# Kernel tuning notes

Measured on AMD Instinct MI355X. Metric: run time of the kernel, lower is better.

## Reference

```python
import jax, jax.numpy as jnp
import numpy as np

NUM_NODES = 50000
EMB_DIM = 128
PROJ_DIM = 768
HIDDEN = 256
NUM_REL = 16
NUM_BASES = 2
NUM_LAYERS = 3
NUM_EDGES = 400000
BN_EPS = 1e-5


def setup_inputs() -> dict:
    key = jax.random.key(0)
    ks = jax.random.split(key, 32)
    inp = {}
    inp["edge_index"] = jax.random.randint(ks[0], (2, NUM_EDGES), 0, NUM_NODES)
    inp["edge_type"] = jax.random.randint(ks[1], (NUM_EDGES,), 0, NUM_REL)
    inp["emb"] = jax.random.normal(ks[2], (NUM_NODES, EMB_DIM), jnp.float32)
    inp["proj_w"] = jax.random.normal(ks[3], (EMB_DIM, PROJ_DIM), jnp.float32) * 0.02
    inp["proj_b"] = jnp.zeros((PROJ_DIM,), jnp.float32)
    dims_in = [PROJ_DIM, HIDDEN, HIDDEN]
    for l in range(NUM_LAYERS):
        d_in = dims_in[l]
        k0, k1, k2 = jax.random.split(ks[4 + l], 3)
        inp[f"comp{l}"] = jax.random.normal(k0, (NUM_REL, NUM_BASES), jnp.float32)
        inp[f"bases{l}"] = jax.random.normal(k1, (NUM_BASES, d_in, HIDDEN), jnp.float32) * (1.0 / np.sqrt(d_in))
        inp[f"root{l}"] = jax.random.normal(k2, (d_in, HIDDEN), jnp.float32) * (1.0 / np.sqrt(d_in))
        inp[f"bias{l}"] = jnp.zeros((HIDDEN,), jnp.float32)
        inp[f"gamma{l}"] = jnp.ones((HIDDEN,), jnp.float32)
        inp[f"beta{l}"] = jnp.zeros((HIDDEN,), jnp.float32)
    return inp


def _rgcn_conv(x, src, dst, edge_type, comp, bases, root, bias):
    # Basis decomposition: W_r = sum_b comp[r,b] * bases[b]
    # Transform nodes per basis once: [B, N, out]
    h = jnp.einsum('nd,bdo->bno', x, bases)
    c = comp[edge_type]                         # [E, B]
    msg = jnp.einsum('beo,eb->eo', h[:, src, :], c)  # [E, out]
    # PyG RGCNConv uses mean aggregation per relation
    seg = dst * NUM_REL + edge_type             # combined (node, relation) id
    cnt = jax.ops.segment_sum(jnp.ones((msg.shape[0],), x.dtype), seg,
                              num_segments=NUM_NODES * NUM_REL)
    denom = jnp.maximum(cnt[seg], 1.0)
    agg = jax.ops.segment_sum(msg / denom[:, None], dst, num_segments=NUM_NODES)
    return agg + x @ root + bias


def _batchnorm(x, gamma, beta):
    mu = jnp.mean(x, axis=0)
    var = jnp.mean(jnp.square(x - mu), axis=0)  # biased, as in torch BN training
    return (x - mu) * jax.lax.rsqrt(var + BN_EPS) * gamma + beta


def reference(edge_index, edge_type, emb, proj_w, proj_b,
              comp0, bases0, root0, bias0, gamma0, beta0,
              comp1, bases1, root1, bias1, gamma1, beta1,
              comp2, bases2, root2, bias2, gamma2, beta2):
    src, dst = edge_index[0], edge_index[1]
    x = emb / jnp.maximum(jnp.linalg.norm(emb, axis=-1, keepdims=True), 1e-12)
    x = x @ proj_w + proj_b
    layers = [(comp0, bases0, root0, bias0, gamma0, beta0),
              (comp1, bases1, root1, bias1, gamma1, beta1),
              (comp2, bases2, root2, bias2, gamma2, beta2)]
    for (comp, bases, root, bias, gamma, beta) in layers:
        x = _rgcn_conv(x, src, dst, edge_type, comp, bases, root, bias)
        x = _batchnorm(x, gamma, beta)
        x = jax.nn.relu(x)
        # dropout: identity (eval mode / deterministic reference)
    return x
```

## Files before the change

kernel.cpp:

```cpp
#include <hip/hip_runtime.h>
#include <hip/hip_bf16.h>

#define NNODES 50000
#define NREL   16
#define NEDGE  400000
#define BN_EPS 1e-5f
#define M_REAL NNODES
#define M_TILES 391
#define RPX    49
#define SCAN_B 512
#define SCAN_NB ((NNODES + SCAN_B - 1) / SCAN_B)

typedef __attribute__((ext_vector_type(8))) short short8;
typedef __attribute__((ext_vector_type(4))) float f4;

__device__ __forceinline__ float bf2f(unsigned short u) {
    union { unsigned int i; float f; } x; x.i = ((unsigned int)u) << 16; return x.f;
}
__device__ __forceinline__ unsigned short f2bf(float f) {
    __hip_bfloat16 h = __float2bfloat16(f);
    union { __hip_bfloat16 h; unsigned short u; } x; x.h = h; return x.u;
}

__device__ __forceinline__ void g2l16(const unsigned short* g, unsigned short* l) {
    __builtin_amdgcn_global_load_lds(
        (const __attribute__((address_space(1))) unsigned int*)g,
        (__attribute__((address_space(3))) unsigned int*)l,
        16, 0, 0);
}

template<int K>
__global__ __launch_bounds__(256) void gemm3_k(
    const unsigned short* __restrict__ A,
    const unsigned short* __restrict__ WT,
    const float* __restrict__ bias,
    float* __restrict__ y,
    float* __restrict__ bns)
{
    const int lin = blockIdx.x;
    const int xcd = lin & 7;
    const int idx = lin >> 3;
    const int row_blk = xcd * RPX + (idx >> 1);
    const int nt = idx & 1;
    if (row_blk >= M_TILES) return;
    const int tile_m = row_blk * 128;
    const int tile_n = nt * 128;

    __shared__ unsigned short As[128 * 64];
    __shared__ unsigned short Bs[128 * 64];

    const int w = threadIdx.x >> 6;
    const int l = threadIdx.x & 63;
    const int lm = l & 15;
    const int kq = l >> 4;
    const int wm = (w & 1) << 6;
    const int wn = (w >> 1) << 6;

    const int lrow = l >> 3;
    const int chunk = ((l & 7) + 8 - lrow) & 7;
    const unsigned short* srcA[4];
    const unsigned short* srcB[4];
    unsigned short* dstA[4];
    unsigned short* dstB[4];
#pragma unroll
    for (int it = 0; it < 4; ++it) {
        int rt = it * 32 + w * 8 + lrow;
        int rg = tile_m + rt; if (rg >= M_REAL) rg = M_REAL - 1;
        srcA[it] = A  + (size_t)rg * K + chunk * 8;
        srcB[it] = WT + (size_t)(tile_n + rt) * K + chunk * 8;
        dstA[it] = As + (it * 32 + w * 8) * 64;
        dstB[it] = Bs + (it * 32 + w * 8) * 64;
    }

    unsigned aoff[4], boff[4];
#pragma unroll
    for (int mi = 0; mi < 4; ++mi) {
        aoff[mi] = (unsigned)((wm + mi * 16 + lm) * 128 + (((kq + lm) & 7) << 4));
        boff[mi] = (unsigned)((wn + mi * 16 + lm) * 128 + (((kq + lm) & 7) << 4));
    }

    f4 acc[4][4];
#pragma unroll
    for (int mi = 0; mi < 4; ++mi)
#pragma unroll
        for (int ni = 0; ni < 4; ++ni) acc[mi][ni] = (f4){0.f, 0.f, 0.f, 0.f};

    for (int kc = 0; kc < K; kc += 64) {
#pragma unroll
        for (int it = 0; it < 4; ++it) {
            g2l16(srcA[it] + kc, dstA[it]);
            g2l16(srcB[it] + kc, dstB[it]);
        }
        __syncthreads();
#pragma unroll
        for (int kh = 0; kh < 2; ++kh) {
            const unsigned x = kh << 6;
            short8 af[4], bfr[4];
#pragma unroll
            for (int mi = 0; mi < 4; ++mi)
                af[mi] = *(const short8*)((const char*)As + (aoff[mi] ^ x));
#pragma unroll
            for (int ni = 0; ni < 4; ++ni)
                bfr[ni] = *(const short8*)((const char*)Bs + (boff[ni] ^ x));
#pragma unroll
            for (int mi = 0; mi < 4; ++mi)
#pragma unroll
                for (int ni = 0; ni < 4; ++ni)
                    acc[mi][ni] = __builtin_amdgcn_mfma_f32_16x16x32_bf16(
                        af[mi], bfr[ni], acc[mi][ni], 0, 0, 0);
        }
        __syncthreads();
    }

    int cols[4]; float bv[4];
#pragma unroll
    for (int ni = 0; ni < 4; ++ni) {
        cols[ni] = tile_n + wn + ni * 16 + lm;
        bv[ni] = bias[cols[ni]];
    }
    float s1[4] = {0.f, 0.f, 0.f, 0.f}, s2[4] = {0.f, 0.f, 0.f, 0.f};
#pragma unroll
    for (int mi = 0; mi < 4; ++mi) {
#pragma unroll
        for (int rg = 0; rg < 4; ++rg) {
            int row = tile_m + wm + mi * 16 + kq * 4 + rg;
            if (row < M_REAL) {
                size_t base = (size_t)row * 256;
#pragma unroll
                for (int ni = 0; ni < 4; ++ni) {
                    float v = acc[mi][ni][rg] + bv[ni];
                    y[base + cols[ni]] = v;
                    s1[ni] += v; s2[ni] += v * v;
                }
            }
        }
    }
#pragma unroll
    for (int ni = 0; ni < 4; ++ni) {
        float a = s1[ni], b = s2[ni];
        a += __shfl_xor(a, 16); a += __shfl_xor(a, 32);
        b += __shfl_xor(b, 16); b += __shfl_xor(b, 32);
        if (l < 16) {
            atomicAdd(&bns[cols[ni]], a);
            atomicAdd(&bns[256 + cols[ni]], b);
        }
    }
}

template<int D, bool HAST>
__global__ __launch_bounds__(256) void gatheru_k(
    unsigned short* buf, const float* __restrict__ comp,
    const unsigned int* __restrict__ rowptr, const float2* __restrict__ erec)
{
    constexpr int E = D / 64;
    constexpr int S = 3 * D + (HAST ? 64 : 0);
    __shared__ float scomp[32];
    if (threadIdx.x < 32) scomp[threadIdx.x] = comp[threadIdx.x];
    __syncthreads();
    int node = blockIdx.x * 4 + (threadIdx.x >> 6);
    int lane = threadIdx.x & 63;
    unsigned int p0 = rowptr[node], p1 = rowptr[node + 1];
    const unsigned short* xbase = buf + 2 * D + lane * E;

    float a0[E], a1[E], b0[E], b1[E];
#pragma unroll
    for (int e = 0; e < E; ++e) { a0[e] = a1[e] = b0[e] = b1[e] = 0.f; }
    float t0 = 0.f, t1 = 0.f;

    unsigned int p = p0;
    for (; p + 4 <= p1; p += 4) {
        float2 r[4];
        unsigned short v[4][E];
#pragma unroll
        for (int j = 0; j < 4; ++j) r[j] = erec[p + j];
#pragma unroll
        for (int j = 0; j < 4; ++j) {
            unsigned q = __float_as_uint(r[j].x);
            const unsigned short* s = xbase + (size_t)(q >> 4) * S;
            if (E == 2) { ushort2 t = *(const ushort2*)s; v[j][0] = t.x; v[j][1] = t.y; }
            else        { ushort4 t = *(const ushort4*)s; v[j][0] = t.x; v[j][1] = t.y;
                          v[j][2] = t.z; v[j][3] = t.w; }
        }
#pragma unroll
        for (int j = 0; j < 4; ++j) {
            unsigned q = __float_as_uint(r[j].x);
            float w0 = scomp[(q & 15) * 2] * r[j].y;
            float w1 = scomp[(q & 15) * 2 + 1] * r[j].y;
            if (HAST) { t0 += w0; t1 += w1; }
            float* d0 = (j & 1) ? b0 : a0;
            float* d1 = (j & 1) ? b1 : a1;
#pragma unroll
            for (int e = 0; e < E; ++e) {
                float xv = bf2f(v[j][e]);
                d0[e] += w0 * xv;
                d1[e] += w1 * xv;
            }
        }
    }
    for (; p < p1; ++p) {
        float2 r = erec[p];
        unsigned q = __float_as_uint(r.x);
        const unsigned short* s = xbase + (size_t)(q >> 4) * S;
        unsigned short v[E];
        if (E == 2) { ushort2 t = *(const ushort2*)s; v[0] = t.x; v[1] = t.y; }
        else        { ushort4 t = *(const ushort4*)s; v[0] = t.x; v[1] = t.y;
                      v[2] = t.z; v[3] = t.w; }
        float w0 = scomp[(q & 15) * 2] * r.y;
        float w1 = scomp[(q & 15) * 2 + 1] * r.y;
        if (HAST) { t0 += w0; t1 += w1; }
#pragma unroll
        for (int e = 0; e < E; ++e) {
            float xv = bf2f(v[e]);
            a0[e] += w0 * xv;
            a1[e] += w1 * xv;
        }
    }

    unsigned short* orow = buf + (size_t)node * S;
    if (E == 2) {
        ushort2 o0, o1;
        o0.x = f2bf(a0[0] + b0[0]); o0.y = f2bf(a0[1] + b0[1]);
        o1.x = f2bf(a1[0] + b1[0]); o1.y = f2bf(a1[1] + b1[1]);
        *(ushort2*)(orow + lane * 2) = o0;
        *(ushort2*)(orow + D + lane * 2) = o1;
    } else {
        ushort4 o0, o1;
        o0.x = f2bf(a0[0] + b0[0]); o0.y = f2bf(a0[1] + b0[1]);
        o0.z = f2bf(a0[2] + b0[2]); o0.w = f2bf(a0[3] + b0[3]);
        o1.x = f2bf(a1[0] + b1[0]); o1.y = f2bf(a1[1] + b1[1]);
        o1.z = f2bf(a1[2] + b1[2]); o1.w = f2bf(a1[3] + b1[3]);
        *(ushort4*)(orow + lane * 4) = o0;
        *(ushort4*)(orow + D + lane * 4) = o1;
    }
    if (HAST) {
        unsigned short tv = (lane == 0) ? f2bf(t0) : (lane == 1) ? f2bf(t1) : (unsigned short)0;
        orow[3 * D + lane] = tv;
    }
}

__global__ __launch_bounds__(256) void norm_k(const float* __restrict__ emb,
                                              unsigned short* __restrict__ buf)
{
    int node = blockIdx.x * 4 + (threadIdx.x >> 6);
    int lane = threadIdx.x & 63;
    const float2* p = (const float2*)(emb + (size_t)node * 128);
    float2 v = p[lane];
    float ss = v.x * v.x + v.y * v.y;
#pragma unroll
    for (int o = 32; o > 0; o >>= 1) ss += __shfl_xor(ss, o);
    float inv = 1.f / fmaxf(sqrtf(ss), 1e-12f);
    unsigned short* row = buf + (size_t)node * 448 + 256;
    unsigned int pack = (unsigned int)f2bf(v.x * inv) | ((unsigned int)f2bf(v.y * inv) << 16);
    ((unsigned int*)row)[lane] = pack;
}

__global__ void zero_k(unsigned int* __restrict__ cnt, unsigned int* __restrict__ cntd,
                       unsigned int* __restrict__ cursor, float* __restrict__ bns)
{
    int i = blockIdx.x * 256 + threadIdx.x;
    if (i < 800000) cnt[i] = 0u;
    if (i < 50000) { cntd[i] = 0u; cursor[i] = 0u; }
    if (i < 1536) bns[i] = 0.f;
}

__global__ void cnt_k(const int* __restrict__ ei, const int* __restrict__ et,
                      unsigned int* __restrict__ cnt, unsigned int* __restrict__ cntd)
{
    int e = blockIdx.x * 256 + threadIdx.x;
    if (e >= NEDGE) return;
    int dst = ei[NEDGE + e];
    atomicAdd(&cnt[(size_t)dst * NREL + et[e]], 1u);
    atomicAdd(&cntd[dst], 1u);
}

__global__ __launch_bounds__(SCAN_B) void scan1_k(const unsigned int* __restrict__ cntd,
                                                  unsigned int* __restrict__ partial,
                                                  unsigned int* __restrict__ bsum)
{
    __shared__ unsigned int s[SCAN_B];
    int i = blockIdx.x * SCAN_B + threadIdx.x;
    unsigned int v = (i < NNODES) ? cntd[i] : 0u;
    s[threadIdx.x] = v;
    __syncthreads();
    for (int off = 1; off < SCAN_B; off <<= 1) {
        unsigned int t = (threadIdx.x >= off) ? s[threadIdx.x - off] : 0u;
        __syncthreads();
        s[threadIdx.x] += t;
        __syncthreads();
    }
    if (i < NNODES) partial[i] = s[threadIdx.x];
    if (threadIdx.x == SCAN_B - 1) bsum[blockIdx.x] = s[SCAN_B - 1];
}

__global__ __launch_bounds__(128) void scan2_k(unsigned int* __restrict__ bsum)
{
    __shared__ unsigned int s[128];
    unsigned int v = (threadIdx.x < SCAN_NB) ? bsum[threadIdx.x] : 0u;
    s[threadIdx.x] = v;
    __syncthreads();
    for (int off = 1; off < 128; off <<= 1) {
        unsigned int t = (threadIdx.x >= off) ? s[threadIdx.x - off] : 0u;
        __syncthreads();
        s[threadIdx.x] += t;
        __syncthreads();
    }
    if (threadIdx.x < SCAN_NB) bsum[threadIdx.x] = s[threadIdx.x];
}

__global__ __launch_bounds__(SCAN_B) void scan3_k(const unsigned int* __restrict__ partial,
                                                  const unsigned int* __restrict__ bsum,
                                                  unsigned int* __restrict__ rowptr)
{
    int i = blockIdx.x * SCAN_B + threadIdx.x;
    if (i >= NNODES) return;
    unsigned int off = (blockIdx.x > 0) ? bsum[blockIdx.x - 1] : 0u;
    rowptr[i + 1] = partial[i] + off;
    if (i == 0) rowptr[0] = 0u;
}

__global__ void fill_k(const int* __restrict__ ei, const int* __restrict__ et,
                       const unsigned int* __restrict__ cnt,
                       const unsigned int* __restrict__ rowptr,
                       unsigned int* __restrict__ cursor,
                       float2* __restrict__ erec)
{
    int e = blockIdx.x * 256 + threadIdx.x;
    if (e >= NEDGE) return;
    int dst = ei[NEDGE + e];
    int t = et[e];
    unsigned int c = cnt[(size_t)dst * NREL + t];
    unsigned int pos = rowptr[dst] + atomicAdd(&cursor[dst], 1u);
    float2 r;
    r.x = __uint_as_float(((unsigned)ei[e] << 4) | (unsigned)t);
    r.y = 1.f / (float)(c ? c : 1u);
    erec[pos] = r;
}

__global__ __launch_bounds__(128) void pt_k(const float* __restrict__ proj_w,
                                            float* __restrict__ PT)
{
    int j = blockIdx.x, d = threadIdx.x;
    PT[(size_t)j * 128 + d] = proj_w[(size_t)d * 768 + j];
}

__global__ __launch_bounds__(128) void pm_k(
    const float* __restrict__ PT, const float* __restrict__ pb,
    const float* __restrict__ b0, const float* __restrict__ r0,
    const float* __restrict__ bias0,
    unsigned short* __restrict__ wTm0, float* __restrict__ biasM0)
{
    __shared__ float sw[128];
    __shared__ float spb[128];
    __shared__ float red[2];
    int seg = blockIdx.x >> 8;
    int n = blockIdx.x & 255;
    int d = threadIdx.x;
    float acc = 0.f, accb = 0.f;
    for (int ch = 0; ch < 6; ++ch) {
        int j0 = ch * 128;
        __syncthreads();
        int j = j0 + d;
        float wv;
        if (seg == 0)      wv = b0[(size_t)j * 256 + n];
        else if (seg == 1) wv = b0[768 * 256 + (size_t)j * 256 + n];
        else               wv = r0[(size_t)j * 256 + n];
        sw[d] = wv;
        spb[d] = pb[j];
        __syncthreads();
#pragma unroll 8
        for (int jj = 0; jj < 128; ++jj)
            acc += PT[(size_t)(j0 + jj) * 128 + d] * sw[jj];
        accb += spb[d] * sw[d];
    }
    for (int o = 32; o > 0; o >>= 1) accb += __shfl_xor(accb, o);
    if ((d & 63) == 0) red[d >> 6] = accb;
    __syncthreads();
    float tb = red[0] + red[1];
    wTm0[(size_t)n * 448 + seg * 128 + d] = f2bf(acc);
    if (seg == 0) { if (d == 0) wTm0[(size_t)n * 448 + 384] = f2bf(tb); }
    else if (seg == 1) { if (d == 0) wTm0[(size_t)n * 448 + 385] = f2bf(tb); }
    else {
        if (d == 0) biasM0[n] = tb + bias0[n];
        if (d >= 2 && d < 64) wTm0[(size_t)n * 448 + 384 + d] = 0;
    }
}

__global__ __launch_bounds__(256) void prep_k(
    const float* __restrict__ b1, const float* __restrict__ r1, const float* __restrict__ bias1,
    const float* __restrict__ b2, const float* __restrict__ r2, const float* __restrict__ bias2,
    unsigned short* __restrict__ wTm1, unsigned short* __restrict__ wTm2,
    float* __restrict__ biasM1, float* __restrict__ biasM2)
{
    int b = blockIdx.x;
    int n = threadIdx.x;
    if (b < 1536) {
        int layer = b / 768;
        int rem = b % 768;
        int seg = rem / 256;
        int k = rem % 256;
        const float* bb = layer ? b2 : b1;
        const float* rr = layer ? r2 : r1;
        const float* in = (seg < 2) ? (bb + (size_t)seg * 256 * 256) : rr;
        unsigned short* out = layer ? wTm2 : wTm1;
        out[(size_t)n * 768 + seg * 256 + k] = f2bf(in[(size_t)k * 256 + n]);
    } else {
        int layer = b - 1536;
        float* bm = layer ? biasM2 : biasM1;
        const float* bs = layer ? bias2 : bias1;
        bm[n] = bs[n];
    }
}

__global__ void bnfin_k(const float* __restrict__ bnsum, const float* __restrict__ gamma,
                        const float* __restrict__ beta, float* __restrict__ bnss)
{
    int c = threadIdx.x;
    float mu = bnsum[c] * (1.f / M_REAL);
    float var = bnsum[256 + c] * (1.f / M_REAL) - mu * mu;
    var = fmaxf(var, 0.f);
    float inv = rsqrtf(var + BN_EPS);
    float sc = gamma[c] * inv;
    bnss[c] = sc;
    bnss[256 + c] = beta[c] - mu * sc;
}

template<bool LAST>
__global__ __launch_bounds__(256) void apply_k(const float* __restrict__ y,
                                               const float* __restrict__ bnss,
                                               unsigned short* __restrict__ xn,
                                               float* __restrict__ outp)
{
    int i = blockIdx.x * 256 + threadIdx.x;
    int row = i >> 6;
    int c4 = (i & 63) * 4;
    f4 v = *(const f4*)(y + (size_t)row * 256 + c4);
    f4 sc = *(const f4*)(bnss + c4);
    f4 sh = *(const f4*)(bnss + 256 + c4);
    f4 r;
    r.x = fmaxf(v.x * sc.x + sh.x, 0.f);
    r.y = fmaxf(v.y * sc.y + sh.y, 0.f);
    r.z = fmaxf(v.z * sc.z + sh.z, 0.f);
    r.w = fmaxf(v.w * sc.w + sh.w, 0.f);
    if (LAST) {
        *(f4*)(outp + (size_t)row * 256 + c4) = r;
    } else {
        ushort4 u;
        u.x = f2bf(r.x); u.y = f2bf(r.y); u.z = f2bf(r.z); u.w = f2bf(r.w);
        *(ushort4*)(xn + (size_t)row * 768 + 512 + c4) = u;
    }
}

extern "C" void kernel_launch(void* const* d_in, const int* in_sizes, int n_in,
                              void* d_out, int out_size, void* d_ws, size_t ws_size,
                              hipStream_t stream)
{
    const int*   edge_index = (const int*)d_in[0];
    const int*   edge_type  = (const int*)d_in[1];
    const float* emb    = (const float*)d_in[2];
    const float* proj_w = (const float*)d_in[3];
    const float* proj_b = (const float*)d_in[4];
    const float* comp[3]  = {(const float*)d_in[5],  (const float*)d_in[11], (const float*)d_in[17]};
    const float* bases[3] = {(const float*)d_in[6],  (const float*)d_in[12], (const float*)d_in[18]};
    const float* root[3]  = {(const float*)d_in[7],  (const float*)d_in[13], (const float*)d_in[19]};
    const float* biasp[3] = {(const float*)d_in[8],  (const float*)d_in[14], (const float*)d_in[20]};
    const float* gamma[3] = {(const float*)d_in[9],  (const float*)d_in[15], (const float*)d_in[21]};
    const float* beta[3]  = {(const float*)d_in[10], (const float*)d_in[16], (const float*)d_in[22]};

    char* ws = (char*)d_ws;
    size_t off = 0;
    auto alloc = [&](size_t bytes) -> char* {
        char* p = ws + off;
        off = (off + bytes + 255) & ~(size_t)255;
        return p;
    };

    unsigned short* axl0 = (unsigned short*)alloc((size_t)NNODES * 448 * 2);
    unsigned short* axl1 = (unsigned short*)alloc((size_t)NNODES * 768 * 2);
    unsigned short* axl2 = (unsigned short*)alloc((size_t)NNODES * 768 * 2);
    float*          y    = (float*)alloc((size_t)NNODES * 256 * 4);
    unsigned int*   cnt  = (unsigned int*)alloc((size_t)NNODES * NREL * 4);
    unsigned int*   cntd = (unsigned int*)alloc((size_t)NNODES * 4);
    unsigned int*   rowptr = (unsigned int*)alloc((size_t)(NNODES + 1) * 4);
    unsigned int*   cursor = (unsigned int*)alloc((size_t)NNODES * 4);
    unsigned int*   partial = (unsigned int*)alloc((size_t)NNODES * 4);
    unsigned int*   bsum = (unsigned int*)alloc(128 * 4);
    float2*         erec = (float2*)alloc((size_t)NEDGE * 8);
    float*          PT   = (float*)alloc((size_t)768 * 128 * 4);
    unsigned short* wTm0 = (unsigned short*)alloc((size_t)256 * 448 * 2);
    unsigned short* wTm1 = (unsigned short*)alloc((size_t)256 * 768 * 2);
    unsigned short* wTm2 = (unsigned short*)alloc((size_t)256 * 768 * 2);
    float* biasM = (float*)alloc(3 * 256 * 4);
    float* bns   = (float*)alloc(3 * 512 * 4);
    float* bnss  = (float*)alloc(3 * 512 * 4);

    zero_k<<<3125, 256, 0, stream>>>(cnt, cntd, cursor, bns);
    norm_k<<<NNODES / 4, 256, 0, stream>>>(emb, axl0);
    cnt_k<<<(NEDGE + 255) / 256, 256, 0, stream>>>(edge_index, edge_type, cnt, cntd);
    scan1_k<<<SCAN_NB, SCAN_B, 0, stream>>>(cntd, partial, bsum);
    scan2_k<<<1, 128, 0, stream>>>(bsum);
    scan3_k<<<SCAN_NB, SCAN_B, 0, stream>>>(partial, bsum, rowptr);
    fill_k<<<(NEDGE + 255) / 256, 256, 0, stream>>>(edge_index, edge_type, cnt, rowptr,
                                                    cursor, erec);

    pt_k<<<768, 128, 0, stream>>>(proj_w, PT);
    pm_k<<<768, 128, 0, stream>>>(PT, proj_b, bases[0], root[0], biasp[0], wTm0, biasM);
    prep_k<<<1538, 256, 0, stream>>>(bases[1], root[1], biasp[1],
                                     bases[2], root[2], biasp[2],
                                     wTm1, wTm2, biasM + 256, biasM + 512);

    gatheru_k<128, true><<<NNODES / 4, 256, 0, stream>>>(axl0, comp[0], rowptr, erec);
    gemm3_k<448><<<8 * RPX * 2, 256, 0, stream>>>(axl0, wTm0, biasM, y, bns);
    bnfin_k<<<1, 256, 0, stream>>>(bns, gamma[0], beta[0], bnss);
    apply_k<false><<<(NNODES * 64) / 256, 256, 0, stream>>>(y, bnss, axl1, nullptr);

    gatheru_k<256, false><<<NNODES / 4, 256, 0, stream>>>(axl1, comp[1], rowptr, erec);
    gemm3_k<768><<<8 * RPX * 2, 256, 0, stream>>>(axl1, wTm1, biasM + 256, y, bns + 512);
    bnfin_k<<<1, 256, 0, stream>>>(bns + 512, gamma[1], beta[1], bnss + 512);
    apply_k<false><<<(NNODES * 64) / 256, 256, 0, stream>>>(y, bnss + 512, axl2, nullptr);

    gatheru_k<256, false><<<NNODES / 4, 256, 0, stream>>>(axl2, comp[2], rowptr, erec);
    gemm3_k<768><<<8 * RPX * 2, 256, 0, stream>>>(axl2, wTm2, biasM + 512, y, bns + 1024);
    bnfin_k<<<1, 256, 0, stream>>>(bns + 1024, gamma[2], beta[2], bnss + 1024);
    apply_k<true><<<(NNODES * 64) / 256, 256, 0, stream>>>(y, bnss + 1024, nullptr, (float*)d_out);
}
```

Measured before the change: 528.4 us.

## Fuse BatchNorm finalize and apply into GEMM via grid-wide barrier

The GEMM kernel now keeps its biased outputs in registers, accumulates the BN statistics, waits at a grid-wide atomic barrier, then applies BN scale/shift and ReLU and writes bf16 (or the final fp32 output) directly. This removes the fp32 intermediate y write and read plus two extra launches per layer. The barrier requires all 784 blocks to be co-resident (launch bounds raised to 4 blocks per CU), and otherwise it could deadlock. Keeping accumulators live across the barrier may also raise register pressure.

```diff
diff --git a/kernel.cpp b/kernel.cpp
--- a/kernel.cpp
+++ b/kernel.cpp
@@ -8,6 +8,7 @@
 #define M_REAL NNODES
 #define M_TILES 391
 #define RPX    49
+#define GRIDB  (8 * RPX * 2)
 #define SCAN_B 512
 #define SCAN_NB ((NNODES + SCAN_B - 1) / SCAN_B)
 
@@ -29,20 +30,24 @@
         16, 0, 0);
 }
 
-template<int K>
-__global__ __launch_bounds__(256) void gemm3_k(
+template<int K, bool LAST>
+__global__ __launch_bounds__(256, 4) void gemmf_k(
     const unsigned short* __restrict__ A,
     const unsigned short* __restrict__ WT,
     const float* __restrict__ bias,
-    float* __restrict__ y,
-    float* __restrict__ bns)
+    float* __restrict__ bns,
+    const float* __restrict__ gamma,
+    const float* __restrict__ beta,
+    unsigned short* __restrict__ xn,
+    float* __restrict__ outp,
+    unsigned int* __restrict__ bar)
 {
     const int lin = blockIdx.x;
     const int xcd = lin & 7;
     const int idx = lin >> 3;
     const int row_blk = xcd * RPX + (idx >> 1);
     const int nt = idx & 1;
-    if (row_blk >= M_TILES) return;
+    const bool active = (row_blk < M_TILES);
     const int tile_m = row_blk * 128;
     const int tile_n = nt * 128;
 
@@ -56,93 +61,140 @@
     const int wm = (w & 1) << 6;
     const int wn = (w >> 1) << 6;
 
-    const int lrow = l >> 3;
-    const int chunk = ((l & 7) + 8 - lrow) & 7;
-    const unsigned short* srcA[4];
-    const unsigned short* srcB[4];
-    unsigned short* dstA[4];
-    unsigned short* dstB[4];
-#pragma unroll
-    for (int it = 0; it < 4; ++it) {
-        int rt = it * 32 + w * 8 + lrow;
-        int rg = tile_m + rt; if (rg >= M_REAL) rg = M_REAL - 1;
-        srcA[it] = A  + (size_t)rg * K + chunk * 8;
-        srcB[it] = WT + (size_t)(tile_n + rt) * K + chunk * 8;
-        dstA[it] = As + (it * 32 + w * 8) * 64;
-        dstB[it] = Bs + (it * 32 + w * 8) * 64;
-    }
-
-    unsigned aoff[4], boff[4];
-#pragma unroll
-    for (int mi = 0; mi < 4; ++mi) {
-        aoff[mi] = (unsigned)((wm + mi * 16 + lm) * 128 + (((kq + lm) & 7) << 4));
-        boff[mi] = (unsigned)((wn + mi * 16 + lm) * 128 + (((kq + lm) & 7) << 4));
-    }
-
     f4 acc[4][4];
 #pragma unroll
     for (int mi = 0; mi < 4; ++mi)
 #pragma unroll
         for (int ni = 0; ni < 4; ++ni) acc[mi][ni] = (f4){0.f, 0.f, 0.f, 0.f};
 
-    for (int kc = 0; kc < K; kc += 64) {
+    int cols[4];
+
+    if (active) {
+        const int lrow = l >> 3;
+        const int chunk = ((l & 7) + 8 - lrow) & 7;
+        const unsigned short* srcA[4];
+        const unsigned short* srcB[4];
+        unsigned short* dstA[4];
+        unsigned short* dstB[4];
 #pragma unroll
         for (int it = 0; it < 4; ++it) {
-            g2l16(srcA[it] + kc, dstA[it]);
-            g2l16(srcB[it] + kc, dstB[it]);
-        }
-        __syncthreads();
-#pragma unroll
-        for (int kh = 0; kh < 2; ++kh) {
-            const unsigned x = kh << 6;
-            short8 af[4], bfr[4];
-#pragma unroll
-            for (int mi = 0; mi < 4; ++mi)
-                af[mi] = *(const short8*)((const char*)As + (aoff[mi] ^ x));
-#pragma unroll
-            for (int ni = 0; ni < 4; ++ni)
-                bfr[ni] = *(const short8*)((const char*)Bs + (boff[ni] ^ x));
-#pragma unroll
-            for (int mi = 0; mi < 4; ++mi)
+            int rt = it * 32 + w * 8 + lrow;
+            int rg = tile_m + rt; if (rg >= M_REAL) rg = M_REAL - 1;
+            srcA[it] = A  + (size_t)rg * K + chunk * 8;
+            srcB[it] = WT + (size_t)(tile_n + rt) * K + chunk * 8;
+            dstA[it] = As + (it * 32 + w * 8) * 64;
+            dstB[it] = Bs + (it * 32 + w * 8) * 64;
+        }
+
+        unsigned aoff[4], boff[4];
+#pragma unroll
+        for (int mi = 0; mi < 4; ++mi) {
+            aoff[mi] = (unsigned)((wm + mi * 16 + lm) * 128 + (((kq + lm) & 7) << 4));
+            boff[mi] = (unsigned)((wn + mi * 16 + lm) * 128 + (((kq + lm) & 7) << 4));
+        }
+
+        for (int kc = 0; kc < K; kc += 64) {
+#pragma unroll
+            for (int it = 0; it < 4; ++it) {
+                g2l16(srcA[it] + kc, dstA[it]);
+                g2l16(srcB[it] + kc, dstB[it]);
+            }
+            __syncthreads();
+#pragma unroll
+            for (int kh = 0; kh < 2; ++kh) {
+                const unsigned x = kh << 6;
+                short8 af[4], bfr[4];
+#pragma unroll
+                for (int mi = 0; mi < 4; ++mi)
+                    af[mi] = *(const short8*)((const char*)As + (aoff[mi] ^ x));
 #pragma unroll
                 for (int ni = 0; ni < 4; ++ni)
-                    acc[mi][ni] = __builtin_amdgcn_mfma_f32_16x16x32_bf16(
-                        af[mi], bfr[ni], acc[mi][ni], 0, 0, 0);
-        }
-        __syncthreads();
-    }
-
-    int cols[4]; float bv[4];
-#pragma unroll
-    for (int ni = 0; ni < 4; ++ni) {
-        cols[ni] = tile_n + wn + ni * 16 + lm;
-        bv[ni] = bias[cols[ni]];
-    }
-    float s1[4] = {0.f, 0.f, 0.f, 0.f}, s2[4] = {0.f, 0.f, 0.f, 0.f};
-#pragma unroll
-    for (int mi = 0; mi < 4; ++mi) {
-#pragma unroll
-        for (int rg = 0; rg < 4; ++rg) {
-            int row = tile_m + wm + mi * 16 + kq * 4 + rg;
-            if (row < M_REAL) {
-                size_t base = (size_t)row * 256;
-#pragma unroll
-                for (int ni = 0; ni < 4; ++ni) {
-                    float v = acc[mi][ni][rg] + bv[ni];
-                    y[base + cols[ni]] = v;
-                    s1[ni] += v; s2[ni] += v * v;
+                    bfr[ni] = *(const short8*)((const char*)Bs + (boff[ni] ^ x));
+#pragma unroll
+                for (int mi = 0; mi < 4; ++mi)
+#pragma unroll
+                    for (int ni = 0; ni < 4; ++ni)
+                        acc[mi][ni] = __builtin_amdgcn_mfma_f32_16x16x32_bf16(
+                            af[mi], bfr[ni], acc[mi][ni], 0, 0, 0);
+            }
+            __syncthreads();
+        }
+
+        float bv[4];
+#pragma unroll
+        for (int ni = 0; ni < 4; ++ni) {
+            cols[ni] = tile_n + wn + ni * 16 + lm;
+            bv[ni] = bias[cols[ni]];
+        }
+        float s1[4] = {0.f, 0.f, 0.f, 0.f}, s2[4] = {0.f, 0.f, 0.f, 0.f};
+#pragma unroll
+        for (int mi = 0; mi < 4; ++mi) {
+#pragma unroll
+            for (int rg = 0; rg < 4; ++rg) {
+                int row = tile_m + wm + mi * 16 + kq * 4 + rg;
+                if (row < M_REAL) {
+#pragma unroll
+                    for (int ni = 0; ni < 4; ++ni) {
+                        float v = acc[mi][ni][rg] + bv[ni];
+                        acc[mi][ni][rg] = v;
+                        s1[ni] += v; s2[ni] += v * v;
+                    }
                 }
             }
         }
-    }
-#pragma unroll
-    for (int ni = 0; ni < 4; ++ni) {
-        float a = s1[ni], b = s2[ni];
-        a += __shfl_xor(a, 16); a += __shfl_xor(a, 32);
-        b += __shfl_xor(b, 16); b += __shfl_xor(b, 32);
-        if (l < 16) {
-            atomicAdd(&bns[cols[ni]], a);
-            atomicAdd(&bns[256 + cols[ni]], b);
+#pragma unroll
+        for (int ni = 0; ni < 4; ++ni) {
+            float a = s1[ni], b = s2[ni];
+            a += __shfl_xor(a, 16); a += __shfl_xor(a, 32);
+            b += __shfl_xor(b, 16); b += __shfl_xor(b, 32);
+            if (l < 16) {
+                atomicAdd(&bns[cols[ni]], a);
+                atomicAdd(&bns[256 + cols[ni]], b);
+            }
+        }
+    }
+
+    __syncthreads();
+    if (threadIdx.x == 0) {
+        __threadfence();
+        __hip_atomic_fetch_add(bar, 1u, __ATOMIC_ACQ_REL, __HIP_MEMORY_SCOPE_AGENT);
+        while (__hip_atomic_load(bar, __ATOMIC_ACQUIRE, __HIP_MEMORY_SCOPE_AGENT)
+               < (unsigned int)GRIDB) {
+            __builtin_amdgcn_s_sleep(8);
+        }
+    }
+    __syncthreads();
+
+    if (active) {
+        const float inv_m = 1.f / (float)M_REAL;
+        float sc[4], sh[4];
+#pragma unroll
+        for (int ni = 0; ni < 4; ++ni) {
+            float t1 = __hip_atomic_load(&bns[cols[ni]], __ATOMIC_RELAXED,
+                                         __HIP_MEMORY_SCOPE_AGENT);
+            float t2 = __hip_atomic_load(&bns[256 + cols[ni]], __ATOMIC_RELAXED,
+                                         __HIP_MEMORY_SCOPE_AGENT);
+            float m1 = t1 * inv_m;
+            float var = t2 * inv_m - m1 * m1;
+            var = fmaxf(var, 0.f);
+            float inv = rsqrtf(var + BN_EPS);
+            sc[ni] = gamma[cols[ni]] * inv;
+            sh[ni] = beta[cols[ni]] - m1 * sc[ni];
+        }
+#pragma unroll
+        for (int mi = 0; mi < 4; ++mi) {
+#pragma unroll
+            for (int rg = 0; rg < 4; ++rg) {
+                int row = tile_m + wm + mi * 16 + kq * 4 + rg;
+                if (row < M_REAL) {
+#pragma unroll
+                    for (int ni = 0; ni < 4; ++ni) {
+                        float r = fmaxf(acc[mi][ni][rg] * sc[ni] + sh[ni], 0.f);
+                        if (LAST) outp[(size_t)row * 256 + cols[ni]] = r;
+                        else      xn[(size_t)row * 768 + 512 + cols[ni]] = f2bf(r);
+                    }
+                }
+            }
         }
     }
 }
@@ -255,12 +307,14 @@
 }
 
 __global__ void zero_k(unsigned int* __restrict__ cnt, unsigned int* __restrict__ cntd,
-                       unsigned int* __restrict__ cursor, float* __restrict__ bns)
+                       unsigned int* __restrict__ cursor, float* __restrict__ bns,
+                       unsigned int* __restrict__ bar)
 {
     int i = blockIdx.x * 256 + threadIdx.x;
     if (i < 800000) cnt[i] = 0u;
     if (i < 50000) { cntd[i] = 0u; cursor[i] = 0u; }
     if (i < 1536) bns[i] = 0.f;
+    if (i < 3) bar[i] = 0u;
 }
 
 __global__ void cnt_k(const int* __restrict__ ei, const int* __restrict__ et,
@@ -411,45 +465,6 @@
     }
 }
 
-__global__ void bnfin_k(const float* __restrict__ bnsum, const float* __restrict__ gamma,
-                        const float* __restrict__ beta, float* __restrict__ bnss)
-{
-    int c = threadIdx.x;
-    float mu = bnsum[c] * (1.f / M_REAL);
-    float var = bnsum[256 + c] * (1.f / M_REAL) - mu * mu;
-    var = fmaxf(var, 0.f);
-    float inv = rsqrtf(var + BN_EPS);
-    float sc = gamma[c] * inv;
-    bnss[c] = sc;
-    bnss[256 + c] = beta[c] - mu * sc;
-}
-
-template<bool LAST>
-__global__ __launch_bounds__(256) void apply_k(const float* __restrict__ y,
-                                               const float* __restrict__ bnss,
-                                               unsigned short* __restrict__ xn,
-                                               float* __restrict__ outp)
-{
-    int i = blockIdx.x * 256 + threadIdx.x;
-    int row = i >> 6;
-    int c4 = (i & 63) * 4;
-    f4 v = *(const f4*)(y + (size_t)row * 256 + c4);
-    f4 sc = *(const f4*)(bnss + c4);
-    f4 sh = *(const f4*)(bnss + 256 + c4);
-    f4 r;
-    r.x = fmaxf(v.x * sc.x + sh.x, 0.f);
-    r.y = fmaxf(v.y * sc.y + sh.y, 0.f);
-    r.z = fmaxf(v.z * sc.z + sh.z, 0.f);
-    r.w = fmaxf(v.w * sc.w + sh.w, 0.f);
-    if (LAST) {
-        *(f4*)(outp + (size_t)row * 256 + c4) = r;
-    } else {
-        ushort4 u;
-        u.x = f2bf(r.x); u.y = f2bf(r.y); u.z = f2bf(r.z); u.w = f2bf(r.w);
-        *(ushort4*)(xn + (size_t)row * 768 + 512 + c4) = u;
-    }
-}
-
 extern "C" void kernel_launch(void* const* d_in, const int* in_sizes, int n_in,
                               void* d_out, int out_size, void* d_ws, size_t ws_size,
                               hipStream_t stream)
@@ -477,7 +492,6 @@
     unsigned short* axl0 = (unsigned short*)alloc((size_t)NNODES * 448 * 2);
     unsigned short* axl1 = (unsigned short*)alloc((size_t)NNODES * 768 * 2);
     unsigned short* axl2 = (unsigned short*)alloc((size_t)NNODES * 768 * 2);
-    float*          y    = (float*)alloc((size_t)NNODES * 256 * 4);
     unsigned int*   cnt  = (unsigned int*)alloc((size_t)NNODES * NREL * 4);
     unsigned int*   cntd = (unsigned int*)alloc((size_t)NNODES * 4);
     unsigned int*   rowptr = (unsigned int*)alloc((size_t)(NNODES + 1) * 4);
@@ -491,9 +505,9 @@
     unsigned short* wTm2 = (unsigned short*)alloc((size_t)256 * 768 * 2);
     float* biasM = (float*)alloc(3 * 256 * 4);
     float* bns   = (float*)alloc(3 * 512 * 4);
-    float* bnss  = (float*)alloc(3 * 512 * 4);
-
-    zero_k<<<3125, 256, 0, stream>>>(cnt, cntd, cursor, bns);
+    unsigned int* bar = (unsigned int*)alloc(3 * 4);
+
+    zero_k<<<3125, 256, 0, stream>>>(cnt, cntd, cursor, bns, bar);
     norm_k<<<NNODES / 4, 256, 0, stream>>>(emb, axl0);
     cnt_k<<<(NEDGE + 255) / 256, 256, 0, stream>>>(edge_index, edge_type, cnt, cntd);
     scan1_k<<<SCAN_NB, SCAN_B, 0, stream>>>(cntd, partial, bsum);
@@ -509,17 +523,14 @@
                                      wTm1, wTm2, biasM + 256, biasM + 512);
 
     gatheru_k<128, true><<<NNODES / 4, 256, 0, stream>>>(axl0, comp[0], rowptr, erec);
-    gemm3_k<448><<<8 * RPX * 2, 256, 0, stream>>>(axl0, wTm0, biasM, y, bns);
-    bnfin_k<<<1, 256, 0, stream>>>(bns, gamma[0], beta[0], bnss);
-    apply_k<false><<<(NNODES * 64) / 256, 256, 0, stream>>>(y, bnss, axl1, nullptr);
+    gemmf_k<448, false><<<GRIDB, 256, 0, stream>>>(axl0, wTm0, biasM, bns,
+                                                   gamma[0], beta[0], axl1, nullptr, bar);
 
     gatheru_k<256, false><<<NNODES / 4, 256, 0, stream>>>(axl1, comp[1], rowptr, erec);
-    gemm3_k<768><<<8 * RPX * 2, 256, 0, stream>>>(axl1, wTm1, biasM + 256, y, bns + 512);
-    bnfin_k<<<1, 256, 0, stream>>>(bns + 512, gamma[1], beta[1], bnss + 512);
-    apply_k<false><<<(NNODES * 64) / 256, 256, 0, stream>>>(y, bnss + 512, axl2, nullptr);
+    gemmf_k<768, false><<<GRIDB, 256, 0, stream>>>(axl1, wTm1, biasM + 256, bns + 512,
+                                                   gamma[1], beta[1], axl2, nullptr, bar + 1);
 
     gatheru_k<256, false><<<NNODES / 4, 256, 0, stream>>>(axl2, comp[2], rowptr, erec);
-    gemm3_k<768><<<8 * RPX * 2, 256, 0, stream>>>(axl2, wTm2, biasM + 512, y, bns + 1024);
-    bnfin_k<<<1, 256, 0, stream>>>(bns + 1024, gamma[2], beta[2], bnss + 1024);
-    apply_k<true><<<(NNODES * 64) / 256, 256, 0, stream>>>(y, bnss + 1024, nullptr, (float*)d_out);
-}
+    gemmf_k<768, true><<<GRIDB, 256, 0, stream>>>(axl2, wTm2, biasM + 512, bns + 1024,
+                                                  gamma[2], beta[2], nullptr, (float*)d_out, bar + 2);
+}
```

Result: slower. 992.5 us (+87.8%).
